# Optimization experiments

Hardware: AMD Instinct MI355X
Metric: run time of the kernel (lower is better)

Reference implementation:

```python
import jax, jax.numpy as jnp
import numpy as np

NUM_GRAPHS = 512


def gcn_conv(x, src, dst, w, W, b):
    # PyG GCNConv: add self-loops (weight 1), symmetric deg^{-1/2} normalization
    n = x.shape[0]
    xw = x @ W  # [N, F_out]
    deg = 1.0 + jax.ops.segment_sum(w, dst, num_segments=n)  # self-loop contributes 1
    dinv = jax.lax.rsqrt(deg)
    norm = w * dinv[src] * dinv[dst]  # [E]
    agg = jax.ops.segment_sum(norm[:, None] * xw[src], dst, num_segments=n)
    return agg + (dinv * dinv)[:, None] * xw + b  # self-loop term = xw / deg


def gap(h, batch, num_graphs):
    s = jax.ops.segment_sum(h, batch, num_segments=num_graphs)
    cnt = jax.ops.segment_sum(jnp.ones((h.shape[0],), h.dtype), batch, num_segments=num_graphs)
    return s / jnp.clip(cnt, 1.0)[:, None]


def setup_inputs() -> dict:
    key = jax.random.key(0)
    ks = jax.random.split(key, 40)
    Nl, El, Ns, Es = 100000, 1600000, 50000, 800000
    Cin_l, Cin_s, H, L1, L2 = 64, 32, 128, 128, 64
    inp = {}
    inp['x_l'] = jax.random.normal(ks[0], (Nl, Cin_l), jnp.float32)
    inp['edge_index_l'] = jax.random.randint(ks[1], (2, El), 0, Nl)
    inp['edge_weight_l'] = jax.random.uniform(ks[2], (El,), jnp.float32)
    inp['x_s'] = jax.random.normal(ks[3], (Ns, Cin_s), jnp.float32)
    inp['edge_index_s'] = jax.random.randint(ks[4], (2, Es), 0, Ns)
    inp['edge_weight_s'] = jax.random.uniform(ks[5], (Es,), jnp.float32)
    inp['batch_index_l'] = jnp.sort(jax.random.randint(ks[6], (Nl,), 0, NUM_GRAPHS))
    inp['batch_index_s'] = jnp.sort(jax.random.randint(ks[7], (Ns,), 0, NUM_GRAPHS))

    def lin(k, fi, fo):
        s = 1.0 / np.sqrt(fi)
        kw, kb = jax.random.split(k)
        return (jax.random.uniform(kw, (fi, fo), jnp.float32, -s, s),
                jax.random.uniform(kb, (fo,), jnp.float32, -s, s))

    dims_a = [Cin_l, H, H, H, H]
    dims_b = [Cin_s, H, H, H, H]
    for i in range(4):
        inp[f'Wa{i}'], inp[f'ba{i}'] = lin(ks[8 + i], dims_a[i], dims_a[i + 1])
        inp[f'Wb{i}'], inp[f'bb{i}'] = lin(ks[12 + i], dims_b[i], dims_b[i + 1])
    inp['lin1_W'], inp['lin1_b'] = lin(ks[16], H, L1)
    inp['lin2_W'], inp['lin2_b'] = lin(ks[17], L1, L2)
    inp['bn_gamma'] = jnp.ones((L2,), jnp.float32)
    inp['bn_beta'] = jnp.zeros((L2,), jnp.float32)
    inp['out_W'], inp['out_b'] = lin(ks[18], L2, 1)
    return inp


def reference(x_l, edge_index_l, edge_weight_l, x_s, edge_index_s, edge_weight_s,
              batch_index_l, batch_index_s,
              Wa0, ba0, Wb0, bb0, Wa1, ba1, Wb1, bb1,
              Wa2, ba2, Wb2, bb2, Wa3, ba3, Wb3, bb3,
              lin1_W, lin1_b, lin2_W, lin2_b, bn_gamma, bn_beta, out_W, out_b):
    # eval mode: dropout = identity, BatchNorm uses running stats (mean 0, var 1)
    sl, dl = edge_index_l[0], edge_index_l[1]
    ss, ds = edge_index_s[0], edge_index_s[1]
    h1 = x_l
    for W, b in ((Wa0, ba0), (Wa1, ba1), (Wa2, ba2), (Wa3, ba3)):
        h1 = jax.nn.relu(gcn_conv(h1, sl, dl, edge_weight_l, W, b))
    h2 = x_s
    for W, b in ((Wb0, bb0), (Wb1, bb1), (Wb2, bb2), (Wb3, bb3)):
        h2 = jax.nn.relu(gcn_conv(h2, ss, ds, edge_weight_s, W, b))
    h = jnp.concatenate([h1, h2], axis=0)
    batch = jnp.concatenate([batch_index_l, batch_index_s], axis=0)
    h = gap(h, batch, NUM_GRAPHS)  # [B, 128]
    h = h @ lin1_W + lin1_b
    h = h @ lin2_W + lin2_b
    eps = 1e-5
    h = (h - 0.0) * jax.lax.rsqrt(jnp.asarray(1.0 + eps)) * bn_gamma + bn_beta
    h = jax.nn.relu(h)
    out = h @ out_W + out_b
    return out, h
```

## Files before the change

### kernel.cpp

```cpp
#include <hip/hip_runtime.h>


static inline size_t align256(size_t x) { return (x + 255) & ~size_t(255); }

__device__ inline unsigned short f2bf(float f) {
    unsigned u = __float_as_uint(f);
    unsigned r = (u + 0x7fffu + ((u >> 16) & 1u)) >> 16;
    return (unsigned short)r;
}
__device__ inline unsigned packbf2(float lo, float hi) {
    return (unsigned)f2bf(lo) | ((unsigned)f2bf(hi) << 16);
}

typedef __attribute__((ext_vector_type(8))) short short8;
typedef __attribute__((ext_vector_type(4))) float floatx4;

#define CHUNK 4096

__global__ __launch_bounds__(256) void bucket_hist(const int* __restrict__ dst, int E,
                                                   int NB, int* __restrict__ bhist) {
    __shared__ int hist[512];
    int t = threadIdx.x;
    for (int i = t; i < NB; i += 256) hist[i] = 0;
    __syncthreads();
    int base = blockIdx.x * CHUNK;
    int end = min(E, base + CHUNK);
    for (int e = base + t; e < end; e += 256) atomicAdd(&hist[dst[e] >> 8], 1);
    __syncthreads();
    for (int i = t; i < NB; i += 256) {
        int h = hist[i];
        if (h > 0) atomicAdd(&bhist[i], h);
    }
}

__global__ __launch_bounds__(256) void scan_buckets(const int* __restrict__ bhist, int nb,
                                                    int* __restrict__ bbase,
                                                    int* __restrict__ bcur,
                                                    int* __restrict__ rp, int N, int E) {
    __shared__ int wsum[4];
    int t = threadIdx.x;
    int wave = t >> 6, lane = t & 63;
    int i0 = 2 * t, i1 = 2 * t + 1;
    int v0 = (i0 < nb) ? bhist[i0] : 0;
    int v1 = (i1 < nb) ? bhist[i1] : 0;
    int tsum = v0 + v1;
    int x = tsum;
    #pragma unroll
    for (int off = 1; off < 64; off <<= 1) {
        int y = __shfl_up(x, off, 64);
        if (lane >= off) x += y;
    }
    if (lane == 63) wsum[wave] = x;
    __syncthreads();
    int woff = 0;
    #pragma unroll
    for (int i = 0; i < 3; i++) if (wave > i) woff += wsum[i];
    int texcl = woff + x - tsum;
    if (i0 < nb) { bbase[i0] = texcl; bcur[i0] = texcl; }
    if (i1 < nb) { bbase[i1] = texcl + v0; bcur[i1] = texcl + v0; }
    if (t == 255) { bbase[nb] = woff + x; rp[N] = E; }
}

__global__ __launch_bounds__(256) void partition_edges(
    const int* __restrict__ src, const int* __restrict__ dst,
    const float* __restrict__ w, int E, int NB,
    int* __restrict__ bcur, int2* __restrict__ part) {
    __shared__ int hist[512];
    __shared__ int lcur[512];
    int t = threadIdx.x;
    for (int i = t; i < NB; i += 256) hist[i] = 0;
    __syncthreads();
    int base = blockIdx.x * CHUNK;
    int end = min(E, base + CHUNK);
    for (int e = base + t; e < end; e += 256) atomicAdd(&hist[dst[e] >> 8], 1);
    __syncthreads();
    for (int i = t; i < NB; i += 256) {
        int h = hist[i];
        if (h > 0) lcur[i] = atomicAdd(&bcur[i], h);
    }
    __syncthreads();
    for (int e = base + t; e < end; e += 256) {
        int d = dst[e];
        int b = d >> 8;
        int pos = atomicAdd(&lcur[b], 1);
        part[pos] = make_int2(src[e] | ((d & 255) << 24), __float_as_int(w[e]));
    }
}

__global__ __launch_bounds__(256) void bucket_csr(
    const int2* __restrict__ part, const int* __restrict__ bbase, int N,
    int* __restrict__ rp, float* __restrict__ dinv, int2* __restrict__ csr) {
    __shared__ int hist[256];
    __shared__ float degw[256];
    __shared__ int wsum[4];
    int b = blockIdx.x, t = threadIdx.x;
    int node0 = b << 8;
    int nn = min(256, N - node0);
    int ebase = bbase[b], eend = bbase[b + 1];
    hist[t] = 0;
    degw[t] = 0.f;
    __syncthreads();
    for (int e = ebase + t; e < eend; e += 256) {
        int2 rec = part[e];
        int nloc = ((unsigned)rec.x) >> 24;
        atomicAdd(&hist[nloc], 1);
        atomicAdd(&degw[nloc], __int_as_float(rec.y));
    }
    __syncthreads();
    int v = hist[t];
    int x = v;
    int wave = t >> 6, lane = t & 63;
    #pragma unroll
    for (int off = 1; off < 64; off <<= 1) {
        int y = __shfl_up(x, off, 64);
        if (lane >= off) x += y;
    }
    if (lane == 63) wsum[wave] = x;
    __syncthreads();
    int woff = 0;
    #pragma unroll
    for (int i = 0; i < 3; i++) if (wave > i) woff += wsum[i];
    int excl = woff + x - v;
    if (t < nn) {
        rp[node0 + t] = ebase + excl;
        dinv[node0 + t] = rsqrtf(1.f + degw[t]);
    }
    hist[t] = excl;
    __syncthreads();
    for (int e = ebase + t; e < eend; e += 256) {
        int2 rec = part[e];
        int nloc = ((unsigned)rec.x) >> 24;
        int pos = ebase + atomicAdd(&hist[nloc], 1);
        csr[pos] = make_int2(rec.x & 0x00FFFFFF, rec.y);
    }
}

template <int F8>
__global__ void cast_bf16_scaled(const float* __restrict__ in, size_t n8,
                                 const float* __restrict__ dinv,
                                 unsigned short* __restrict__ out) {
    size_t i = (size_t)blockIdx.x * blockDim.x + threadIdx.x;
    if (i >= n8) return;
    float s = dinv[i / F8];
    const float4* in4 = (const float4*)in;
    float4 a = in4[i * 2], b = in4[i * 2 + 1];
    ushort4 lo, hi;
    lo.x = f2bf(a.x * s); lo.y = f2bf(a.y * s); lo.z = f2bf(a.z * s); lo.w = f2bf(a.w * s);
    hi.x = f2bf(b.x * s); hi.y = f2bf(b.y * s); hi.z = f2bf(b.z * s); hi.w = f2bf(b.w * s);
    ushort4* o4 = (ushort4*)out;
    o4[i * 2] = lo;
    o4[i * 2 + 1] = hi;
}

struct WCastArgs {
    const float* w[8];
    unsigned short* o[8];
    int K[8];
};
__global__ void cast_w16t(WCastArgs p) {
    int mi = blockIdx.y;
    int K = p.K[mi];
    int id = blockIdx.x * 256 + threadIdx.x;
    if (id >= K * 128) return;
    int k = id >> 7, c = id & 127;
    p.o[mi][c * K + k] = f2bf(p.w[mi][k * 128 + c]);
}

template <int LANES>
__global__ void aggregate_bf16(const unsigned short* __restrict__ h16, int N,
                               const int* __restrict__ rp,
                               const int2* __restrict__ csr,
                               const float* __restrict__ dinv,
                               unsigned short* __restrict__ z16) {
    constexpr int GPB = 256 / LANES;
    int group = threadIdx.x / LANES;
    int lane = threadIdx.x % LANES;
    int n = blockIdx.x * GPB + group;
    if (n >= N) return;
    const uint4* h4 = (const uint4*)h16;
    float acc[8];
    #pragma unroll
    for (int i = 0; i < 8; i++) acc[i] = 0.f;

    int e = rp[n], end = rp[n + 1];
    for (; e + 3 < end; e += 4) {
        int2 c0 = csr[e], c1 = csr[e + 1], c2 = csr[e + 2], c3 = csr[e + 3];
        uint4 q0 = h4[(size_t)c0.x * LANES + lane];
        uint4 q1 = h4[(size_t)c1.x * LANES + lane];
        uint4 q2 = h4[(size_t)c2.x * LANES + lane];
        uint4 q3 = h4[(size_t)c3.x * LANES + lane];
        float n0 = __int_as_float(c0.y), n1 = __int_as_float(c1.y);
        float n2 = __int_as_float(c2.y), n3 = __int_as_float(c3.y);
        #define ACC8(q, nm)                                                   \
        {                                                                     \
            acc[0] += nm * __uint_as_float(q.x << 16);                        \
            acc[1] += nm * __uint_as_float(q.x & 0xffff0000u);                \
            acc[2] += nm * __uint_as_float(q.y << 16);                        \
            acc[3] += nm * __uint_as_float(q.y & 0xffff0000u);                \
            acc[4] += nm * __uint_as_float(q.z << 16);                        \
            acc[5] += nm * __uint_as_float(q.z & 0xffff0000u);                \
            acc[6] += nm * __uint_as_float(q.w << 16);                        \
            acc[7] += nm * __uint_as_float(q.w & 0xffff0000u);                \
        }
        ACC8(q0, n0) ACC8(q1, n1) ACC8(q2, n2) ACC8(q3, n3)
    }
    for (; e < end; e++) {
        int2 c = csr[e];
        uint4 q = h4[(size_t)c.x * LANES + lane];
        float nm = __int_as_float(c.y);
        ACC8(q, nm)
    }
    uint4 qs = h4[(size_t)n * LANES + lane];
    float di = dinv[n];
    float v0 = (acc[0] + __uint_as_float(qs.x << 16)) * di;
    float v1 = (acc[1] + __uint_as_float(qs.x & 0xffff0000u)) * di;
    float v2 = (acc[2] + __uint_as_float(qs.y << 16)) * di;
    float v3 = (acc[3] + __uint_as_float(qs.y & 0xffff0000u)) * di;
    float v4 = (acc[4] + __uint_as_float(qs.z << 16)) * di;
    float v5 = (acc[5] + __uint_as_float(qs.z & 0xffff0000u)) * di;
    float v6 = (acc[6] + __uint_as_float(qs.w << 16)) * di;
    float v7 = (acc[7] + __uint_as_float(qs.w & 0xffff0000u)) * di;
    uint4 o;
    o.x = packbf2(v0, v1); o.y = packbf2(v2, v3);
    o.z = packbf2(v4, v5); o.w = packbf2(v6, v7);
    *(uint4*)&z16[(size_t)n * (LANES * 8) + lane * 8] = o;
    #undef ACC8
}

template <int K>
__global__ __launch_bounds__(256) void gemm_mfma(
    const unsigned short* __restrict__ Z16, const unsigned short* __restrict__ WT16,
    const float* __restrict__ bias, const float* __restrict__ dinv,
    float* __restrict__ Hf, unsigned short* __restrict__ H16, int N) {
    constexpr int KP = K + 8;
    __shared__ __attribute__((aligned(16))) unsigned short WT[128 * KP];
    int tid = threadIdx.x;
    constexpr int CH = 128 * K / 8;
    for (int i = tid; i < CH; i += 256) {
        int c = i / (K / 8), kc = i % (K / 8);
        *(uint4*)&WT[c * KP + kc * 8] = *(const uint4*)&WT16[c * K + kc * 8];
    }
    __syncthreads();

    int wave = tid >> 6, lane = tid & 63;
    int m = lane & 15, quad = lane >> 4;
    int rowbase = blockIdx.x * 128 + wave * 32;

    floatx4 acc[2][8];
    #pragma unroll
    for (int t = 0; t < 2; t++)
        #pragma unroll
        for (int ct = 0; ct < 8; ct++) acc[t][ct] = (floatx4)0.f;

    for (int ks = 0; ks < K; ks += 32) {
        short8 a[2];
        #pragma unroll
        for (int t = 0; t < 2; t++) {
            int r = rowbase + t * 16 + m;
            short8 av = (short8)0;
            if (r < N) av = *(const short8*)&Z16[(size_t)r * K + ks + quad * 8];
            a[t] = av;
        }
        #pragma unroll
        for (int ct = 0; ct < 8; ct++) {
            short8 b = *(const short8*)&WT[(ct * 16 + m) * KP + ks + quad * 8];
            acc[0][ct] = __builtin_amdgcn_mfma_f32_16x16x32_bf16(a[0], b, acc[0][ct], 0, 0, 0);
            acc[1][ct] = __builtin_amdgcn_mfma_f32_16x16x32_bf16(a[1], b, acc[1][ct], 0, 0, 0);
        }
    }

    float bv[8];
    #pragma unroll
    for (int ct = 0; ct < 8; ct++) bv[ct] = bias[ct * 16 + m];

    #pragma unroll
    for (int t = 0; t < 2; t++) {
        #pragma unroll
        for (int reg = 0; reg < 4; reg++) {
            int r = rowbase + t * 16 + quad * 4 + reg;
            if (r >= N) continue;
            float di = H16 ? dinv[r] : 1.f;
            #pragma unroll
            for (int ct = 0; ct < 8; ct++) {
                float o = fmaxf(acc[t][ct][reg] + bv[ct], 0.f);
                size_t off = (size_t)r * 128 + ct * 16 + m;
                if (H16) H16[off] = f2bf(o * di);
                if (Hf) Hf[off] = o;
            }
        }
    }
}

__global__ __launch_bounds__(256) void pool_accum(const float* __restrict__ h,
                                                  const int* __restrict__ batch, int N,
                                                  float* __restrict__ psum) {
    int tid = threadIdx.x;
    int f4 = tid & 31;
    int nl = tid >> 5;
    int n0 = blockIdx.x * 256 + nl;
    const float4* h4 = (const float4*)h;
    float4 acc = make_float4(0.f, 0.f, 0.f, 0.f);
    int cur = -1;
    #pragma unroll 4
    for (int i = 0; i < 32; i++) {
        int n = n0 + i * 8;
        if (n >= N) break;
        int g = batch[n];
        if (g != cur) {
            if (cur >= 0) {
                float* d = &psum[(size_t)cur * 128 + f4 * 4];
                atomicAdd(d + 0, acc.x);
                atomicAdd(d + 1, acc.y);
                atomicAdd(d + 2, acc.z);
                atomicAdd(d + 3, acc.w);
            }
            cur = g;
            acc = make_float4(0.f, 0.f, 0.f, 0.f);
        }
        float4 v = h4[(size_t)n * 32 + f4];
        acc.x += v.x; acc.y += v.y; acc.z += v.z; acc.w += v.w;
    }
    if (cur >= 0) {
        float* d = &psum[(size_t)cur * 128 + f4 * 4];
        atomicAdd(d + 0, acc.x);
        atomicAdd(d + 1, acc.y);
        atomicAdd(d + 2, acc.z);
        atomicAdd(d + 3, acc.w);
    }
}

__device__ inline int lower_bound(const int* __restrict__ a, int n, int v) {
    int lo = 0, hi = n;
    while (lo < hi) {
        int m = (lo + hi) >> 1;
        if (a[m] < v) lo = m + 1; else hi = m;
    }
    return lo;
}

__global__ void mlp_kernel(const float* __restrict__ psum,
                           const int* __restrict__ batchL, int NL,
                           const int* __restrict__ batchS, int NS,
                           const float* __restrict__ W1, const float* __restrict__ b1,
                           const float* __restrict__ W2, const float* __restrict__ b2,
                           const float* __restrict__ gamma, const float* __restrict__ beta,
                           const float* __restrict__ outW, const float* __restrict__ outb,
                           float* __restrict__ d_out) {
    __shared__ float row[128];
    __shared__ float row2[128];
    int g = blockIdx.x, t = threadIdx.x;
    int cnt = (lower_bound(batchL, NL, g + 1) - lower_bound(batchL, NL, g)) +
              (lower_bound(batchS, NS, g + 1) - lower_bound(batchS, NS, g));
    float rcp = 1.f / (float)(cnt > 0 ? cnt : 1);
    row[t] = psum[(size_t)g * 128 + t] * rcp;
    __syncthreads();
    float a = b1[t];
    #pragma unroll 4
    for (int k = 0; k < 128; k++) a += row[k] * W1[k * 128 + t];
    row2[t] = a;
    __syncthreads();
    if (t < 64) {
        float a2 = b2[t];
        #pragma unroll 4
        for (int k = 0; k < 128; k++) a2 += row2[k] * W2[k * 64 + t];
        float rs = rsqrtf(1.0f + 1e-5f);
        float hb = a2 * rs * gamma[t] + beta[t];
        float hr = fmaxf(hb, 0.f);
        d_out[512 + g * 64 + t] = hr;
        float p = hr * outW[t];
        #pragma unroll
        for (int off = 32; off > 0; off >>= 1) p += __shfl_down(p, off, 64);
        if (t == 0) d_out[g] = p + outb[0];
    }
}

extern "C" void kernel_launch(void* const* d_in, const int* in_sizes, int n_in,
                              void* d_out, int out_size, void* d_ws, size_t ws_size,
                              hipStream_t stream) {
    const float* x_l = (const float*)d_in[0];
    const int*   ei_l = (const int*)d_in[1];
    const float* w_l = (const float*)d_in[2];
    const float* x_s = (const float*)d_in[3];
    const int*   ei_s = (const int*)d_in[4];
    const float* w_s = (const float*)d_in[5];
    const int*   batch_l = (const int*)d_in[6];
    const int*   batch_s = (const int*)d_in[7];

    const int NL = in_sizes[6];
    const int NS = in_sizes[7];
    const int EL = in_sizes[2];
    const int ES = in_sizes[5];

    const float* Wa[4] = {(const float*)d_in[8],  (const float*)d_in[12],
                          (const float*)d_in[16], (const float*)d_in[20]};
    const float* ba[4] = {(const float*)d_in[9],  (const float*)d_in[13],
                          (const float*)d_in[17], (const float*)d_in[21]};
    const float* Wb[4] = {(const float*)d_in[10], (const float*)d_in[14],
                          (const float*)d_in[18], (const float*)d_in[22]};
    const float* bb[4] = {(const float*)d_in[11], (const float*)d_in[15],
                          (const float*)d_in[19], (const float*)d_in[23]};
    const float* lin1_W = (const float*)d_in[24];
    const float* lin1_b = (const float*)d_in[25];
    const float* lin2_W = (const float*)d_in[26];
    const float* lin2_b = (const float*)d_in[27];
    const float* bn_g = (const float*)d_in[28];
    const float* bn_b = (const float*)d_in[29];
    const float* out_W = (const float*)d_in[30];
    const float* out_b = (const float*)d_in[31];
    float* out = (float*)d_out;

    const int* src_l = ei_l;
    const int* dst_l = ei_l + EL;
    const int* src_s = ei_s;
    const int* dst_s = ei_s + ES;

    const int NBL = (NL + 255) >> 8;
    const int NBS = (NS + 255) >> 8;

    char* p = (char*)d_ws;
    auto alloc = [&](size_t bytes) { char* r = p; p += align256(bytes); return r; };
    float* A_l = (float*)alloc((size_t)NL * 128 * 4);
    float* A_s = (float*)alloc((size_t)NS * 128 * 4);
    unsigned short* Z16_l = (unsigned short*)alloc((size_t)NL * 128 * 2);
    unsigned short* Z16_s = (unsigned short*)alloc((size_t)NS * 128 * 2);
    unsigned short* H16_l = (unsigned short*)alloc((size_t)NL * 128 * 2);
    unsigned short* H16_s = (unsigned short*)alloc((size_t)NS * 128 * 2);
    int2*  csr_l  = (int2*)alloc((size_t)EL * 8);
    int2*  csr_s  = (int2*)alloc((size_t)ES * 8);
    int2*  part_l = (int2*)alloc((size_t)EL * 8);
    int2*  part_s = (int2*)alloc((size_t)ES * 8);
    int*   rp_l  = (int*)alloc((size_t)(NL + 1) * 4);
    int*   rp_s  = (int*)alloc((size_t)(NS + 1) * 4);
    float* dinv_l = (float*)alloc((size_t)NL * 4);
    float* dinv_s = (float*)alloc((size_t)NS * 4);
    int*   bhist_l = (int*)alloc(512 * 4);
    int*   bhist_s = (int*)alloc(512 * 4);
    int*   bbase_l = (int*)alloc(512 * 4);
    int*   bbase_s = (int*)alloc(512 * 4);
    int*   bcur_l  = (int*)alloc(512 * 4);
    int*   bcur_s  = (int*)alloc(512 * 4);
    float* psum = (float*)alloc((size_t)512 * 128 * 4);
    unsigned short* WTa[4];
    unsigned short* WTb[4];
    WTa[0] = (unsigned short*)alloc((size_t)128 * 64 * 2);
    for (int i = 1; i < 4; i++) WTa[i] = (unsigned short*)alloc((size_t)128 * 128 * 2);
    WTb[0] = (unsigned short*)alloc((size_t)128 * 32 * 2);
    for (int i = 1; i < 4; i++) WTb[i] = (unsigned short*)alloc((size_t)128 * 128 * 2);
    (void)ws_size; (void)n_in; (void)out_size;

    hipMemsetAsync(bhist_l, 0, 512 * 4, stream);
    hipMemsetAsync(bhist_s, 0, 512 * 4, stream);
    hipMemsetAsync(psum, 0, (size_t)512 * 128 * 4, stream);

    {
        WCastArgs wa;
        for (int i = 0; i < 4; i++) {
            wa.w[i] = Wa[i]; wa.o[i] = WTa[i]; wa.K[i] = (i == 0) ? 64 : 128;
            wa.w[4 + i] = Wb[i]; wa.o[4 + i] = WTb[i]; wa.K[4 + i] = (i == 0) ? 32 : 128;
        }
        cast_w16t<<<dim3(64, 8), 256, 0, stream>>>(wa);
    }

    bucket_hist<<<(EL + CHUNK - 1) / CHUNK, 256, 0, stream>>>(dst_l, EL, NBL, bhist_l);
    bucket_hist<<<(ES + CHUNK - 1) / CHUNK, 256, 0, stream>>>(dst_s, ES, NBS, bhist_s);
    scan_buckets<<<1, 256, 0, stream>>>(bhist_l, NBL, bbase_l, bcur_l, rp_l, NL, EL);
    scan_buckets<<<1, 256, 0, stream>>>(bhist_s, NBS, bbase_s, bcur_s, rp_s, NS, ES);
    partition_edges<<<(EL + CHUNK - 1) / CHUNK, 256, 0, stream>>>(src_l, dst_l, w_l, EL,
                                                                  NBL, bcur_l, part_l);
    partition_edges<<<(ES + CHUNK - 1) / CHUNK, 256, 0, stream>>>(src_s, dst_s, w_s, ES,
                                                                  NBS, bcur_s, part_s);
    bucket_csr<<<NBL, 256, 0, stream>>>(part_l, bbase_l, NL, rp_l, dinv_l, csr_l);
    bucket_csr<<<NBS, 256, 0, stream>>>(part_s, bbase_s, NS, rp_s, dinv_s, csr_s);

    {
        size_t n8l = (size_t)NL * 64 / 8;
        size_t n8s = (size_t)NS * 32 / 8;
        cast_bf16_scaled<8><<<(int)((n8l + 255) / 256), 256, 0, stream>>>(x_l, n8l, dinv_l,
                                                                          H16_l);
        cast_bf16_scaled<4><<<(int)((n8s + 255) / 256), 256, 0, stream>>>(x_s, n8s, dinv_s,
                                                                          H16_s);
    }

    const int gmL = (NL + 127) / 128;
    const int gmS = (NS + 127) / 128;

    aggregate_bf16<8><<<(NL + 31) / 32, 256, 0, stream>>>(
        H16_l, NL, rp_l, csr_l, dinv_l, Z16_l);
    gemm_mfma<64><<<gmL, 256, 0, stream>>>(Z16_l, WTa[0], ba[0], dinv_l,
                                           (float*)nullptr, H16_l, NL);
    for (int layer = 1; layer < 4; layer++) {
        aggregate_bf16<16><<<(NL + 15) / 16, 256, 0, stream>>>(
            H16_l, NL, rp_l, csr_l, dinv_l, Z16_l);
        if (layer < 3)
            gemm_mfma<128><<<gmL, 256, 0, stream>>>(Z16_l, WTa[layer], ba[layer], dinv_l,
                                                    (float*)nullptr, H16_l, NL);
        else
            gemm_mfma<128><<<gmL, 256, 0, stream>>>(Z16_l, WTa[layer], ba[layer], dinv_l,
                                                    A_l, (unsigned short*)nullptr, NL);
    }

    aggregate_bf16<4><<<(NS + 63) / 64, 256, 0, stream>>>(
        H16_s, NS, rp_s, csr_s, dinv_s, Z16_s);
    gemm_mfma<32><<<gmS, 256, 0, stream>>>(Z16_s, WTb[0], bb[0], dinv_s,
                                           (float*)nullptr, H16_s, NS);
    for (int layer = 1; layer < 4; layer++) {
        aggregate_bf16<16><<<(NS + 15) / 16, 256, 0, stream>>>(
            H16_s, NS, rp_s, csr_s, dinv_s, Z16_s);
        if (layer < 3)
            gemm_mfma<128><<<gmS, 256, 0, stream>>>(Z16_s, WTb[layer], bb[layer], dinv_s,
                                                    (float*)nullptr, H16_s, NS);
        else
            gemm_mfma<128><<<gmS, 256, 0, stream>>>(Z16_s, WTb[layer], bb[layer], dinv_s,
                                                    A_s, (unsigned short*)nullptr, NS);
    }

    pool_accum<<<(NL + 255) / 256, 256, 0, stream>>>(A_l, batch_l, NL, psum);
    pool_accum<<<(NS + 255) / 256, 256, 0, stream>>>(A_s, batch_s, NS, psum);
    mlp_kernel<<<512, 128, 0, stream>>>(psum, batch_l, NL, batch_s, NS,
                                        lin1_W, lin1_b, lin2_W, lin2_b,
                                        bn_g, bn_b, out_W, out_b, out);
}
```

Baseline: 862.2 us.

## Merge large and small graph branches into dual-dispatch kernels, unroll aggregation by 8

Each pipeline stage (bucket histogram, scan, partition, CSR build, input cast, aggregation, GEMM, pooling) now runs as one launch whose blocks are split between the large and small graphs by block index. This halves the number of launches and lets the small-graph work fill the GPU alongside the large-graph work instead of running serially after it. The aggregation inner loop also gets an 8-edge unrolled path so more gathers are in flight per thread, at the cost of more registers.

```diff
diff --git a/kernel.cpp b/kernel.cpp
--- a/kernel.cpp
+++ b/kernel.cpp
@@ -17,32 +17,43 @@
 
 #define CHUNK 4096
 
-__global__ __launch_bounds__(256) void bucket_hist(const int* __restrict__ dst, int E,
-                                                   int NB, int* __restrict__ bhist) {
+__global__ __launch_bounds__(256) void bucket_hist_dual(
+    const int* __restrict__ dstL, int EL, int NBL, int* __restrict__ bhL,
+    const int* __restrict__ dstS, int ES, int NBS, int* __restrict__ bhS, int CL) {
     __shared__ int hist[512];
-    int t = threadIdx.x;
+    int b = blockIdx.x, t = threadIdx.x;
+    const int* dst; int E, NB, blk; int* bh;
+    if (b < CL) { dst = dstL; E = EL; NB = NBL; bh = bhL; blk = b; }
+    else        { dst = dstS; E = ES; NB = NBS; bh = bhS; blk = b - CL; }
     for (int i = t; i < NB; i += 256) hist[i] = 0;
     __syncthreads();
-    int base = blockIdx.x * CHUNK;
+    int base = blk * CHUNK;
     int end = min(E, base + CHUNK);
     for (int e = base + t; e < end; e += 256) atomicAdd(&hist[dst[e] >> 8], 1);
     __syncthreads();
     for (int i = t; i < NB; i += 256) {
         int h = hist[i];
-        if (h > 0) atomicAdd(&bhist[i], h);
-    }
-}
-
-__global__ __launch_bounds__(256) void scan_buckets(const int* __restrict__ bhist, int nb,
-                                                    int* __restrict__ bbase,
-                                                    int* __restrict__ bcur,
-                                                    int* __restrict__ rp, int N, int E) {
+        if (h > 0) atomicAdd(&bh[i], h);
+    }
+}
+
+__global__ __launch_bounds__(256) void scan_buckets_dual(
+    const int* __restrict__ bhist, int* __restrict__ bbase, int* __restrict__ bcur,
+    int nbL, int* __restrict__ rpL, int NL, int EL,
+    int nbS, int* __restrict__ rpS, int NS, int ES) {
     __shared__ int wsum[4];
-    int t = threadIdx.x;
+    int which = blockIdx.x, t = threadIdx.x;
+    const int* bh = bhist + which * 512;
+    int* bb = bbase + which * 512;
+    int* bc = bcur + which * 512;
+    int nb = which ? nbS : nbL;
+    int* rp = which ? rpS : rpL;
+    int N = which ? NS : NL;
+    int E = which ? ES : EL;
     int wave = t >> 6, lane = t & 63;
     int i0 = 2 * t, i1 = 2 * t + 1;
-    int v0 = (i0 < nb) ? bhist[i0] : 0;
-    int v1 = (i1 < nb) ? bhist[i1] : 0;
+    int v0 = (i0 < nb) ? bh[i0] : 0;
+    int v1 = (i1 < nb) ? bh[i1] : 0;
     int tsum = v0 + v1;
     int x = tsum;
     #pragma unroll
@@ -56,21 +67,29 @@
     #pragma unroll
     for (int i = 0; i < 3; i++) if (wave > i) woff += wsum[i];
     int texcl = woff + x - tsum;
-    if (i0 < nb) { bbase[i0] = texcl; bcur[i0] = texcl; }
-    if (i1 < nb) { bbase[i1] = texcl + v0; bcur[i1] = texcl + v0; }
-    if (t == 255) { bbase[nb] = woff + x; rp[N] = E; }
-}
-
-__global__ __launch_bounds__(256) void partition_edges(
-    const int* __restrict__ src, const int* __restrict__ dst,
-    const float* __restrict__ w, int E, int NB,
-    int* __restrict__ bcur, int2* __restrict__ part) {
+    if (i0 < nb) { bb[i0] = texcl; bc[i0] = texcl; }
+    if (i1 < nb) { bb[i1] = texcl + v0; bc[i1] = texcl + v0; }
+    if (t == 255) { bb[nb] = woff + x; rp[N] = E; }
+}
+
+__global__ __launch_bounds__(256) void partition_edges_dual(
+    const int* __restrict__ srcL, const int* __restrict__ dstL,
+    const float* __restrict__ wL, int EL, int NBL, int* __restrict__ bcurL,
+    int2* __restrict__ partL,
+    const int* __restrict__ srcS, const int* __restrict__ dstS,
+    const float* __restrict__ wS, int ES, int NBS, int* __restrict__ bcurS,
+    int2* __restrict__ partS, int CL) {
     __shared__ int hist[512];
     __shared__ int lcur[512];
-    int t = threadIdx.x;
+    int b = blockIdx.x, t = threadIdx.x;
+    const int *src, *dst; const float* w; int E, NB, blk; int* bcur; int2* part;
+    if (b < CL) { src = srcL; dst = dstL; w = wL; E = EL; NB = NBL; bcur = bcurL;
+                  part = partL; blk = b; }
+    else        { src = srcS; dst = dstS; w = wS; E = ES; NB = NBS; bcur = bcurS;
+                  part = partS; blk = b - CL; }
     for (int i = t; i < NB; i += 256) hist[i] = 0;
     __syncthreads();
-    int base = blockIdx.x * CHUNK;
+    int base = blk * CHUNK;
     int end = min(E, base + CHUNK);
     for (int e = base + t; e < end; e += 256) atomicAdd(&hist[dst[e] >> 8], 1);
     __syncthreads();
@@ -81,19 +100,27 @@
     __syncthreads();
     for (int e = base + t; e < end; e += 256) {
         int d = dst[e];
-        int b = d >> 8;
-        int pos = atomicAdd(&lcur[b], 1);
+        int bk = d >> 8;
+        int pos = atomicAdd(&lcur[bk], 1);
         part[pos] = make_int2(src[e] | ((d & 255) << 24), __float_as_int(w[e]));
     }
 }
 
-__global__ __launch_bounds__(256) void bucket_csr(
-    const int2* __restrict__ part, const int* __restrict__ bbase, int N,
-    int* __restrict__ rp, float* __restrict__ dinv, int2* __restrict__ csr) {
+__global__ __launch_bounds__(256) void bucket_csr_dual(
+    const int2* __restrict__ partL, const int* __restrict__ bbaseL, int NL,
+    int* __restrict__ rpL, float* __restrict__ dinvL, int2* __restrict__ csrL,
+    const int2* __restrict__ partS, const int* __restrict__ bbaseS, int NS,
+    int* __restrict__ rpS, float* __restrict__ dinvS, int2* __restrict__ csrS,
+    int NBL) {
     __shared__ int hist[256];
     __shared__ float degw[256];
     __shared__ int wsum[4];
-    int b = blockIdx.x, t = threadIdx.x;
+    int bb = blockIdx.x, t = threadIdx.x;
+    const int2* part; const int* bbase; int N, b; int* rp; float* dinv; int2* csr;
+    if (bb < NBL) { part = partL; bbase = bbaseL; N = NL; rp = rpL; dinv = dinvL;
+                    csr = csrL; b = bb; }
+    else          { part = partS; bbase = bbaseS; N = NS; rp = rpS; dinv = dinvS;
+                    csr = csrS; b = bb - NBL; }
     int node0 = b << 8;
     int nn = min(256, N - node0);
     int ebase = bbase[b], eend = bbase[b + 1];
@@ -136,10 +163,9 @@
 }
 
 template <int F8>
-__global__ void cast_bf16_scaled(const float* __restrict__ in, size_t n8,
-                                 const float* __restrict__ dinv,
-                                 unsigned short* __restrict__ out) {
-    size_t i = (size_t)blockIdx.x * blockDim.x + threadIdx.x;
+__device__ void cast_body(const float* __restrict__ in, size_t n8,
+                          const float* __restrict__ dinv,
+                          unsigned short* __restrict__ out, size_t i) {
     if (i >= n8) return;
     float s = dinv[i / F8];
     const float4* in4 = (const float4*)in;
@@ -150,6 +176,16 @@
     ushort4* o4 = (ushort4*)out;
     o4[i * 2] = lo;
     o4[i * 2 + 1] = hi;
+}
+
+__global__ void cast0_dual(const float* __restrict__ xL, size_t n8L,
+                           const float* __restrict__ dinvL, unsigned short* __restrict__ oL,
+                           const float* __restrict__ xS, size_t n8S,
+                           const float* __restrict__ dinvS, unsigned short* __restrict__ oS,
+                           int BL) {
+    int b = blockIdx.x;
+    if (b < BL) cast_body<8>(xL, n8L, dinvL, oL, (size_t)b * 256 + threadIdx.x);
+    else        cast_body<4>(xS, n8S, dinvS, oS, (size_t)(b - BL) * 256 + threadIdx.x);
 }
 
 struct WCastArgs {
@@ -167,15 +203,14 @@
 }
 
 template <int LANES>
-__global__ void aggregate_bf16(const unsigned short* __restrict__ h16, int N,
-                               const int* __restrict__ rp,
-                               const int2* __restrict__ csr,
-                               const float* __restrict__ dinv,
-                               unsigned short* __restrict__ z16) {
+__device__ void agg_body(const unsigned short* __restrict__ h16, int N,
+                         const int* __restrict__ rp, const int2* __restrict__ csr,
+                         const float* __restrict__ dinv,
+                         unsigned short* __restrict__ z16, int blk) {
     constexpr int GPB = 256 / LANES;
     int group = threadIdx.x / LANES;
     int lane = threadIdx.x % LANES;
-    int n = blockIdx.x * GPB + group;
+    int n = blk * GPB + group;
     if (n >= N) return;
     const uint4* h4 = (const uint4*)h16;
     float acc[8];
@@ -183,26 +218,42 @@
     for (int i = 0; i < 8; i++) acc[i] = 0.f;
 
     int e = rp[n], end = rp[n + 1];
+    #define ACC8(q, nm)                                                   \
+    {                                                                     \
+        acc[0] += nm * __uint_as_float(q.x << 16);                        \
+        acc[1] += nm * __uint_as_float(q.x & 0xffff0000u);                \
+        acc[2] += nm * __uint_as_float(q.y << 16);                        \
+        acc[3] += nm * __uint_as_float(q.y & 0xffff0000u);                \
+        acc[4] += nm * __uint_as_float(q.z << 16);                        \
+        acc[5] += nm * __uint_as_float(q.z & 0xffff0000u);                \
+        acc[6] += nm * __uint_as_float(q.w << 16);                        \
+        acc[7] += nm * __uint_as_float(q.w & 0xffff0000u);                \
+    }
+    for (; e + 7 < end; e += 8) {
+        int2 c[8];
+        uint4 q[8];
+        #pragma unroll
+        for (int j = 0; j < 8; j++) c[j] = csr[e + j];
+        #pragma unroll
+        for (int j = 0; j < 8; j++) q[j] = h4[(size_t)c[j].x * LANES + lane];
+        #pragma unroll
+        for (int j = 0; j < 8; j++) {
+            float nm = __int_as_float(c[j].y);
+            ACC8(q[j], nm)
+        }
+    }
     for (; e + 3 < end; e += 4) {
-        int2 c0 = csr[e], c1 = csr[e + 1], c2 = csr[e + 2], c3 = csr[e + 3];
-        uint4 q0 = h4[(size_t)c0.x * LANES + lane];
-        uint4 q1 = h4[(size_t)c1.x * LANES + lane];
-        uint4 q2 = h4[(size_t)c2.x * LANES + lane];
-        uint4 q3 = h4[(size_t)c3.x * LANES + lane];
-        float n0 = __int_as_float(c0.y), n1 = __int_as_float(c1.y);
-        float n2 = __int_as_float(c2.y), n3 = __int_as_float(c3.y);
-        #define ACC8(q, nm)                                                   \
-        {                                                                     \
-            acc[0] += nm * __uint_as_float(q.x << 16);                        \
-            acc[1] += nm * __uint_as_float(q.x & 0xffff0000u);                \
-            acc[2] += nm * __uint_as_float(q.y << 16);                        \
-            acc[3] += nm * __uint_as_float(q.y & 0xffff0000u);                \
-            acc[4] += nm * __uint_as_float(q.z << 16);                        \
-            acc[5] += nm * __uint_as_float(q.z & 0xffff0000u);                \
-            acc[6] += nm * __uint_as_float(q.w << 16);                        \
-            acc[7] += nm * __uint_as_float(q.w & 0xffff0000u);                \
+        int2 c[4];
+        uint4 q[4];
+        #pragma unroll
+        for (int j = 0; j < 4; j++) c[j] = csr[e + j];
+        #pragma unroll
+        for (int j = 0; j < 4; j++) q[j] = h4[(size_t)c[j].x * LANES + lane];
+        #pragma unroll
+        for (int j = 0; j < 4; j++) {
+            float nm = __int_as_float(c[j].y);
+            ACC8(q[j], nm)
         }
-        ACC8(q0, n0) ACC8(q1, n1) ACC8(q2, n2) ACC8(q3, n3)
     }
     for (; e < end; e++) {
         int2 c = csr[e];
@@ -227,13 +278,37 @@
     #undef ACC8
 }
 
+__global__ __launch_bounds__(256) void aggregate_dual(
+    const unsigned short* __restrict__ hL, int NL, const int* __restrict__ rpL,
+    const int2* __restrict__ csrL, const float* __restrict__ dinvL,
+    unsigned short* __restrict__ zL,
+    const unsigned short* __restrict__ hS, int NS, const int* __restrict__ rpS,
+    const int2* __restrict__ csrS, const float* __restrict__ dinvS,
+    unsigned short* __restrict__ zS, int gL) {
+    int b = blockIdx.x;
+    if (b < gL) agg_body<16>(hL, NL, rpL, csrL, dinvL, zL, b);
+    else        agg_body<16>(hS, NS, rpS, csrS, dinvS, zS, b - gL);
+}
+
+__global__ __launch_bounds__(256) void aggregate0_dual(
+    const unsigned short* __restrict__ hL, int NL, const int* __restrict__ rpL,
+    const int2* __restrict__ csrL, const float* __restrict__ dinvL,
+    unsigned short* __restrict__ zL,
+    const unsigned short* __restrict__ hS, int NS, const int* __restrict__ rpS,
+    const int2* __restrict__ csrS, const float* __restrict__ dinvS,
+    unsigned short* __restrict__ zS, int gL) {
+    int b = blockIdx.x;
+    if (b < gL) agg_body<8>(hL, NL, rpL, csrL, dinvL, zL, b);
+    else        agg_body<4>(hS, NS, rpS, csrS, dinvS, zS, b - gL);
+}
+
 template <int K>
-__global__ __launch_bounds__(256) void gemm_mfma(
-    const unsigned short* __restrict__ Z16, const unsigned short* __restrict__ WT16,
-    const float* __restrict__ bias, const float* __restrict__ dinv,
-    float* __restrict__ Hf, unsigned short* __restrict__ H16, int N) {
+__device__ void gemm_body(const unsigned short* __restrict__ Z16,
+                          const unsigned short* __restrict__ WT16,
+                          const float* __restrict__ bias, const float* __restrict__ dinv,
+                          float* __restrict__ Hf, unsigned short* __restrict__ H16,
+                          int N, int blk, unsigned short* WT) {
     constexpr int KP = K + 8;
-    __shared__ __attribute__((aligned(16))) unsigned short WT[128 * KP];
     int tid = threadIdx.x;
     constexpr int CH = 128 * K / 8;
     for (int i = tid; i < CH; i += 256) {
@@ -244,7 +319,7 @@
 
     int wave = tid >> 6, lane = tid & 63;
     int m = lane & 15, quad = lane >> 4;
-    int rowbase = blockIdx.x * 128 + wave * 32;
+    int rowbase = blk * 128 + wave * 32;
 
     floatx4 acc[2][8];
     #pragma unroll
@@ -291,13 +366,34 @@
     }
 }
 
-__global__ __launch_bounds__(256) void pool_accum(const float* __restrict__ h,
-                                                  const int* __restrict__ batch, int N,
-                                                  float* __restrict__ psum) {
+template <int K>
+__global__ __launch_bounds__(256) void gemm_mfma(
+    const unsigned short* __restrict__ Z16, const unsigned short* __restrict__ WT16,
+    const float* __restrict__ bias, const float* __restrict__ dinv,
+    float* __restrict__ Hf, unsigned short* __restrict__ H16, int N) {
+    __shared__ __attribute__((aligned(16))) unsigned short WT[128 * (K + 8)];
+    gemm_body<K>(Z16, WT16, bias, dinv, Hf, H16, N, blockIdx.x, WT);
+}
+
+__global__ __launch_bounds__(256) void gemm_mfma_dual128(
+    const unsigned short* __restrict__ ZL, const unsigned short* __restrict__ WTL,
+    const float* __restrict__ bL, const float* __restrict__ dinvL,
+    float* __restrict__ HfL, unsigned short* __restrict__ H16L, int NL,
+    const unsigned short* __restrict__ ZS, const unsigned short* __restrict__ WTS,
+    const float* __restrict__ bS, const float* __restrict__ dinvS,
+    float* __restrict__ HfS, unsigned short* __restrict__ H16S, int NS, int gmL) {
+    __shared__ __attribute__((aligned(16))) unsigned short WT[128 * 136];
+    int b = blockIdx.x;
+    if (b < gmL) gemm_body<128>(ZL, WTL, bL, dinvL, HfL, H16L, NL, b, WT);
+    else         gemm_body<128>(ZS, WTS, bS, dinvS, HfS, H16S, NS, b - gmL, WT);
+}
+
+__device__ void pool_body(const float* __restrict__ h, const int* __restrict__ batch,
+                          int N, float* __restrict__ psum, int blk) {
     int tid = threadIdx.x;
     int f4 = tid & 31;
     int nl = tid >> 5;
-    int n0 = blockIdx.x * 256 + nl;
+    int n0 = blk * 256 + nl;
     const float4* h4 = (const float4*)h;
     float4 acc = make_float4(0.f, 0.f, 0.f, 0.f);
     int cur = -1;
@@ -329,6 +425,15 @@
     }
 }
 
+__global__ __launch_bounds__(256) void pool_dual(
+    const float* __restrict__ hL, const int* __restrict__ bL, int NL,
+    const float* __restrict__ hS, const int* __restrict__ bS, int NS,
+    float* __restrict__ psum, int gL) {
+    int b = blockIdx.x;
+    if (b < gL) pool_body(hL, bL, NL, psum, b);
+    else        pool_body(hS, bS, NS, psum, b - gL);
+}
+
 __device__ inline int lower_bound(const int* __restrict__ a, int n, int v) {
     int lo = 0, hi = n;
     while (lo < hi) {
@@ -416,6 +521,8 @@
 
     const int NBL = (NL + 255) >> 8;
     const int NBS = (NS + 255) >> 8;
+    const int CL = (EL + CHUNK - 1) / CHUNK;
+    const int CS = (ES + CHUNK - 1) / CHUNK;
 
     char* p = (char*)d_ws;
     auto alloc = [&](size_t bytes) { char* r = p; p += align256(bytes); return r; };
@@ -433,12 +540,9 @@
     int*   rp_s  = (int*)alloc((size_t)(NS + 1) * 4);
     float* dinv_l = (float*)alloc((size_t)NL * 4);
     float* dinv_s = (float*)alloc((size_t)NS * 4);
-    int*   bhist_l = (int*)alloc(512 * 4);
-    int*   bhist_s = (int*)alloc(512 * 4);
-    int*   bbase_l = (int*)alloc(512 * 4);
-    int*   bbase_s = (int*)alloc(512 * 4);
-    int*   bcur_l  = (int*)alloc(512 * 4);
-    int*   bcur_s  = (int*)alloc(512 * 4);
+    int*   bhist  = (int*)alloc(1024 * 4);
+    int*   bbase  = (int*)alloc(1024 * 4);
+    int*   bcur   = (int*)alloc(1024 * 4);
     float* psum = (float*)alloc((size_t)512 * 128 * 4);
     unsigned short* WTa[4];
     unsigned short* WTb[4];
@@ -448,8 +552,7 @@
     for (int i = 1; i < 4; i++) WTb[i] = (unsigned short*)alloc((size_t)128 * 128 * 2);
     (void)ws_size; (void)n_in; (void)out_size;
 
-    hipMemsetAsync(bhist_l, 0, 512 * 4, stream);
-    hipMemsetAsync(bhist_s, 0, 512 * 4, stream);
+    hipMemsetAsync(bhist, 0, 1024 * 4, stream);
     hipMemsetAsync(psum, 0, (size_t)512 * 128 * 4, stream);
 
     {
@@ -461,61 +564,57 @@
         cast_w16t<<<dim3(64, 8), 256, 0, stream>>>(wa);
     }
 
-    bucket_hist<<<(EL + CHUNK - 1) / CHUNK, 256, 0, stream>>>(dst_l, EL, NBL, bhist_l);
-    bucket_hist<<<(ES + CHUNK - 1) / CHUNK, 256, 0, stream>>>(dst_s, ES, NBS, bhist_s);
-    scan_buckets<<<1, 256, 0, stream>>>(bhist_l, NBL, bbase_l, bcur_l, rp_l, NL, EL);
-    scan_buckets<<<1, 256, 0, stream>>>(bhist_s, NBS, bbase_s, bcur_s, rp_s, NS, ES);
-    partition_edges<<<(EL + CHUNK - 1) / CHUNK, 256, 0, stream>>>(src_l, dst_l, w_l, EL,
-                                                                  NBL, bcur_l, part_l);
-    partition_edges<<<(ES + CHUNK - 1) / CHUNK, 256, 0, stream>>>(src_s, dst_s, w_s, ES,
-                                                                  NBS, bcur_s, part_s);
-    bucket_csr<<<NBL, 256, 0, stream>>>(part_l, bbase_l, NL, rp_l, dinv_l, csr_l);
-    bucket_csr<<<NBS, 256, 0, stream>>>(part_s, bbase_s, NS, rp_s, dinv_s, csr_s);
-
-    {
-        size_t n8l = (size_t)NL * 64 / 8;
-        size_t n8s = (size_t)NS * 32 / 8;
-        cast_bf16_scaled<8><<<(int)((n8l + 255) / 256), 256, 0, stream>>>(x_l, n8l, dinv_l,
-                                                                          H16_l);
-        cast_bf16_scaled<4><<<(int)((n8s + 255) / 256), 256, 0, stream>>>(x_s, n8s, dinv_s,
-                                                                          H16_s);
-    }
+    bucket_hist_dual<<<CL + CS, 256, 0, stream>>>(dst_l, EL, NBL, bhist,
+                                                  dst_s, ES, NBS, bhist + 512, CL);
+    scan_buckets_dual<<<2, 256, 0, stream>>>(bhist, bbase, bcur,
+                                             NBL, rp_l, NL, EL,
+                                             NBS, rp_s, NS, ES);
+    partition_edges_dual<<<CL + CS, 256, 0, stream>>>(
+        src_l, dst_l, w_l, EL, NBL, bcur, part_l,
+        src_s, dst_s, w_s, ES, NBS, bcur + 512, part_s, CL);
+    bucket_csr_dual<<<NBL + NBS, 256, 0, stream>>>(
+        part_l, bbase, NL, rp_l, dinv_l, csr_l,
+        part_s, bbase + 512, NS, rp_s, dinv_s, csr_s, NBL);
+
+    const size_t n8l = (size_t)NL * 8;
+    const size_t n8s = (size_t)NS * 4;
+    const int cBL = (int)((n8l + 255) / 256);
+    const int cBS = (int)((n8s + 255) / 256);
+    cast0_dual<<<cBL + cBS, 256, 0, stream>>>(x_l, n8l, dinv_l, H16_l,
+                                              x_s, n8s, dinv_s, H16_s, cBL);
 
     const int gmL = (NL + 127) / 128;
     const int gmS = (NS + 127) / 128;
-
-    aggregate_bf16<8><<<(NL + 31) / 32, 256, 0, stream>>>(
-        H16_l, NL, rp_l, csr_l, dinv_l, Z16_l);
+    const int aL = (NL + 15) / 16;
+    const int aS = (NS + 15) / 16;
+    const int a0L = (NL + 31) / 32;
+    const int a0S = (NS + 63) / 64;
+
+    aggregate0_dual<<<a0L + a0S, 256, 0, stream>>>(
+        H16_l, NL, rp_l, csr_l, dinv_l, Z16_l,
+        H16_s, NS, rp_s, csr_s, dinv_s, Z16_s, a0L);
     gemm_mfma<64><<<gmL, 256, 0, stream>>>(Z16_l, WTa[0], ba[0], dinv_l,
                                            (float*)nullptr, H16_l, NL);
-    for (int layer = 1; layer < 4; layer++) {
-        aggregate_bf16<16><<<(NL + 15) / 16, 256, 0, stream>>>(
-            H16_l, NL, rp_l, csr_l, dinv_l, Z16_l);
-        if (layer < 3)
-            gemm_mfma<128><<<gmL, 256, 0, stream>>>(Z16_l, WTa[layer], ba[layer], dinv_l,
-                                                    (float*)nullptr, H16_l, NL);
-        else
-            gemm_mfma<128><<<gmL, 256, 0, stream>>>(Z16_l, WTa[layer], ba[layer], dinv_l,
-                                                    A_l, (unsigned short*)nullptr, NL);
-    }
-
-    aggregate_bf16<4><<<(NS + 63) / 64, 256, 0, stream>>>(
-        H16_s, NS, rp_s, csr_s, dinv_s, Z16_s);
     gemm_mfma<32><<<gmS, 256, 0, stream>>>(Z16_s, WTb[0], bb[0], dinv_s,
                                            (float*)nullptr, H16_s, NS);
+
     for (int layer = 1; layer < 4; layer++) {
-        aggregate_bf16<16><<<(NS + 15) / 16, 256, 0, stream>>>(
-            H16_s, NS, rp_s, csr_s, dinv_s, Z16_s);
+        aggregate_dual<<<aL + aS, 256, 0, stream>>>(
+            H16_l, NL, rp_l, csr_l, dinv_l, Z16_l,
+            H16_s, NS, rp_s, csr_s, dinv_s, Z16_s, aL);
         if (layer < 3)
-            gemm_mfma<128><<<gmS, 256, 0, stream>>>(Z16_s, WTb[layer], bb[layer], dinv_s,
-                                                    (float*)nullptr, H16_s, NS);
+            gemm_mfma_dual128<<<gmL + gmS, 256, 0, stream>>>(
+                Z16_l, WTa[layer], ba[layer], dinv_l, (float*)nullptr, H16_l, NL,
+                Z16_s, WTb[layer], bb[layer], dinv_s, (float*)nullptr, H16_s, NS, gmL);
         else
-            gemm_mfma<128><<<gmS, 256, 0, stream>>>(Z16_s, WTb[layer], bb[layer], dinv_s,
-                                                    A_s, (unsigned short*)nullptr, NS);
-    }
-
-    pool_accum<<<(NL + 255) / 256, 256, 0, stream>>>(A_l, batch_l, NL, psum);
-    pool_accum<<<(NS + 255) / 256, 256, 0, stream>>>(A_s, batch_s, NS, psum);
+            gemm_mfma_dual128<<<gmL + gmS, 256, 0, stream>>>(
+                Z16_l, WTa[layer], ba[layer], dinv_l, A_l, (unsigned short*)nullptr, NL,
+                Z16_s, WTb[layer], bb[layer], dinv_s, A_s, (unsigned short*)nullptr, NS, gmL);
+    }
+
+    const int pL = (NL + 255) / 256;
+    const int pS = (NS + 255) / 256;
+    pool_dual<<<pL + pS, 256, 0, stream>>>(A_l, batch_l, NL, A_s, batch_s, NS, psum, pL);
     mlp_kernel<<<512, 128, 0, stream>>>(psum, batch_l, NL, batch_s, NS,
                                         lin1_W, lin1_b, lin2_W, lin2_b,
                                         bn_g, bn_b, out_W, out_b, out);
```

Result: no change. 863.9 us (+0.2%).
